# Kernel optimization log

Measured on AMD Instinct MI355X. Metric: run time of the kernel, lower is better.

Reference implementation:

```python
import jax, jax.numpy as jnp
import numpy as np
import math

N = 100000
D = 128       # input_dim
DK = 32       # d_k
H = 4         # heads
DV = D // H   # d_v = 32
DFF = 512     # 4 * input_dim
EPS = 1e-5


def layer_norm(x, g, b):
    mu = jnp.mean(x, axis=-1, keepdims=True)
    var = jnp.var(x, axis=-1, keepdims=True)
    return (x - mu) * jax.lax.rsqrt(var + EPS) * g + b


def setup_inputs() -> dict:
    key = jax.random.key(0)
    ks = jax.random.split(key, 10)
    x = jax.random.normal(ks[0], (N, D), dtype=jnp.float32)
    neighbor_index = jax.random.randint(ks[1], (N, 4), 0, N)
    # xavier-ish scaled params
    w_q = jax.random.normal(ks[2], (H, D, DK), dtype=jnp.float32) * math.sqrt(2.0 / (D + DK))
    w_k = jax.random.normal(ks[3], (H, 5, D, DK), dtype=jnp.float32) * math.sqrt(2.0 / (D + DK))
    w_v = jax.random.normal(ks[4], (H, 5, D, DV), dtype=jnp.float32) * math.sqrt(2.0 / (D + DV))
    W1 = jax.random.normal(ks[5], (D, DFF), dtype=jnp.float32) * math.sqrt(1.0 / D)
    b1 = jnp.zeros((DFF,), dtype=jnp.float32)
    W2 = jax.random.normal(ks[6], (DFF, D), dtype=jnp.float32) * math.sqrt(1.0 / DFF)
    b2 = jnp.zeros((D,), dtype=jnp.float32)
    g1 = jnp.ones((D,), dtype=jnp.float32)
    beta1 = jnp.zeros((D,), dtype=jnp.float32)
    g2 = jnp.ones((D,), dtype=jnp.float32)
    beta2 = jnp.zeros((D,), dtype=jnp.float32)
    return {"x": x, "neighbor_index": neighbor_index, "w_q": w_q, "w_k": w_k,
            "w_v": w_v, "W1": W1, "b1": b1, "W2": W2, "b2": b2,
            "g1": g1, "beta1": beta1, "g2": g2, "beta2": beta2}


def attention(x, neighbor_index, w_q, w_k, w_v):
    # gather the 4 typed neighbors and prepend the self node -> (N, 5, D)
    x_nb = jnp.concatenate([x[:, None, :], x[neighbor_index]], axis=1)
    Q = jnp.einsum('nd,hdk->hnk', x, w_q)                 # (H, N, DK)
    K = jnp.einsum('nrd,hrdk->hnrk', x_nb, w_k)           # (H, N, 5, DK)
    V = jnp.einsum('nrd,hrdv->hnrv', x_nb, w_v)           # (H, N, 5, DV)
    A = jnp.einsum('hnk,hnrk->hnr', Q, K) / math.sqrt(DK)
    # NOTE: original torch code applies softmax over dim=1 (the node axis),
    # reproduced faithfully here.
    A = jax.nn.softmax(A, axis=1)
    Z = jnp.einsum('hnr,hnrv->hnv', A, V)                 # (H, N, DV)
    return jnp.transpose(Z, (1, 0, 2)).reshape(x.shape[0], -1)  # (N, H*DV)


def reference(x, neighbor_index, w_q, w_k, w_v, W1, b1, W2, b2, g1, beta1, g2, beta2):
    attn = attention(x, neighbor_index, w_q, w_k, w_v)
    h = layer_norm(x + attn, g1, beta1)
    ffn = jax.nn.relu(h @ W1 + b1) @ W2 + b2
    return layer_norm(h + ffn, g2, beta2)
```

## Files before the change

kernel.cpp:

```cpp
#include <hip/hip_runtime.h>
#include <hip/hip_bf16.h>

typedef unsigned short u16;
typedef __attribute__((ext_vector_type(8))) short short8;
typedef __attribute__((ext_vector_type(4))) float f32x4;
typedef __attribute__((ext_vector_type(4))) float float4v;
typedef __attribute__((ext_vector_type(4))) unsigned short us4;
typedef __attribute__((ext_vector_type(4))) int int4v;

#define NN       100000
#define OFF_WK   16384
#define OFF_WV   98304
#define OFF_W1   180224
#define PACK_ELEMS 311296

#define WS_LWS   0u
#define WS_PM    8000000u
#define WS_PS    8000640u
#define WS_MHR   8001280u
#define WS_ISHR  8001408u
#define WS_PK    8001536u
#define WS_XB    8624128u
#define WS_SV    34224128u

#define PWS_PITCH 40
#define PWS_SLICE 1280

static __device__ __forceinline__ float b2f(u16 u){
  unsigned int i = ((unsigned int)u) << 16;
  float f; __builtin_memcpy(&f, &i, 4); return f;
}
static __device__ __forceinline__ u16 f2b(float f){
  unsigned int i; __builtin_memcpy(&i, &f, 4);
  i += 0x7FFFu + ((i >> 16) & 1u);
  return (u16)(i >> 16);
}
static __device__ __forceinline__ f32x4 mfma16(short8 a, short8 b, f32x4 c){
  return __builtin_amdgcn_mfma_f32_16x16x32_bf16(a, b, c, 0, 0, 0);
}
static __device__ __forceinline__ bool detect32(const void* g1){
  return ((const u16*)g1)[0] == 0;
}
static __device__ __forceinline__ float ldf(const void* p, size_t i, bool is32){
  return is32 ? ((const float*)p)[i] : b2f(((const u16*)p)[i]);
}

static __device__ __forceinline__ void stage32k(
    const u16* __restrict__ g, u16* l, int wv, int lane)
{
  #pragma unroll
  for (int k = 0; k < 8; k++){
    int off = k*4096 + wv*1024;
    __builtin_amdgcn_global_load_lds(
        (const __attribute__((address_space(1))) void*)((const char*)g + off + lane*16),
        (__attribute__((address_space(3))) void*)((char*)l + off),
        16, 0, 0);
  }
}

#define VMW8() asm volatile("s_waitcnt vmcnt(8)" ::: "memory")
#define VMW0() asm volatile("s_waitcnt vmcnt(0)" ::: "memory")
#define SBAR() asm volatile("s_barrier" ::: "memory")

__global__ __launch_bounds__(256) void k_convert_x(
    const void* __restrict__ x, const void* __restrict__ g1, u16* __restrict__ xb)
{
  const bool is32 = detect32(g1);
  size_t i = (size_t)blockIdx.x * 256 + threadIdx.x;
  us4 o;
  if (is32){
    float4v v = ((const float4v*)x)[i];
    o.x = f2b(v.x); o.y = f2b(v.y); o.z = f2b(v.z); o.w = f2b(v.w);
  } else {
    o = ((const us4*)x)[i];
  }
  ((us4*)xb)[i] = o;
}

__global__ __launch_bounds__(256) void k_pack(
    const void* __restrict__ wq, const void* __restrict__ wk,
    const void* __restrict__ wv, const void* __restrict__ W1,
    const void* __restrict__ W2, const void* __restrict__ g1,
    const void* __restrict__ b1, const void* __restrict__ b2,
    const void* __restrict__ be1, const void* __restrict__ g2,
    const void* __restrict__ be2,
    u16* __restrict__ pk, u16* __restrict__ sv)
{
  const bool is32 = detect32(g1);
  int p = blockIdx.x * 256 + threadIdx.x;
  if (p < PACK_ELEMS){
    float v;
    if (p < OFF_WK){
      int q = p;
      int j = q & 7, lane = (q >> 3) & 63, tk = q >> 9;
      int kb = tk & 3, t = tk >> 2;
      int kd = kb*32 + (lane>>4)*8 + j, nc = t*16 + (lane & 15);
      v = ldf(wq, (size_t)(nc>>5)*4096 + kd*32 + (nc & 31), is32);
    } else if (p < OFF_WV){
      int q = p - OFF_WK; int r = q >> 14; q &= 16383;
      int j = q & 7, lane = (q >> 3) & 63, tk = q >> 9;
      int kb = tk & 3, t = tk >> 2;
      int kd = kb*32 + (lane>>4)*8 + j, nc = t*16 + (lane & 15);
      v = ldf(wk, (size_t)((nc>>5)*5 + r)*4096 + kd*32 + (nc & 31), is32);
    } else if (p < OFF_W1){
      int q = p - OFF_WV; int r = q >> 14; q &= 16383;
      int j = q & 7, lane = (q >> 3) & 63, tk = q >> 9;
      int kb = tk & 3, t = tk >> 2;
      int kd = kb*32 + (lane>>4)*8 + j, nc = t*16 + (lane & 15);
      v = ldf(wv, (size_t)((nc>>5)*5 + r)*4096 + kd*32 + (nc & 31), is32);
    } else {
      int q = p - OFF_W1;
      int j = q & 7, lane = (q >> 3) & 63, rest = q >> 9;
      int pairIdx = rest >> 4, sub = rest & 15;
      int c = pairIdx >> 2, kb2 = pairIdx & 3;
      int half = lane >> 4, mc = lane & 15;
      if (sub < 8){
        int u = sub >> 2, kb = sub & 3;
        int kd = kb*32 + half*8 + j;
        int nc = c*128 + (kb2*2+u)*16 + mc;
        v = ldf(W1, (size_t)kd*512 + nc, is32);
      } else {
        int t = sub - 8;
        int kd = (c*4+kb2)*32 + half*8 + j;
        int nc = t*16 + mc;
        v = ldf(W2, (size_t)kd*128 + nc, is32);
      }
    }
    pk[p] = f2b(v);
  }
  if (blockIdx.x == 0){
    for (int i = threadIdx.x; i < 1152; i += 256){
      const void* src; int off;
      if      (i < 512) { src = b1;  off = i; }
      else if (i < 640) { src = b2;  off = i - 512; }
      else if (i < 768) { src = g1;  off = i - 640; }
      else if (i < 896) { src = be1; off = i - 768; }
      else if (i < 1024){ src = g2;  off = i - 896; }
      else              { src = be2; off = i - 1024; }
      sv[i] = f2b(ldf(src, off, is32));
    }
  }
}

__global__ __launch_bounds__(256, 2) void k_qk(
    const u16* __restrict__ x, const int* __restrict__ nbr,
    const u16* __restrict__ pw, float* __restrict__ lws)
{
  __shared__ __align__(16) u16 sbuf[32768];
  const int tid = threadIdx.x, lane = tid & 63, wv = tid >> 6;
  const int m = lane & 15, quad = lane >> 4;
  const int n0 = blockIdx.x * 128 + wv * 32;
  const bool act0 = (n0 < NN), act1 = (n0 + 16 < NN);
  const short8* sb8 = (const short8*)sbuf;

  int nd[2][4];
  short8 a2[2][4], a2n[2][4];
  #pragma unroll
  for (int tl = 0; tl < 2; tl++){
    if (!(tl ? act1 : act0)) continue;
    int4v t4 = *(const int4v*)(nbr + (size_t)(n0 + tl*16 + m)*4);
    nd[tl][0]=t4.x; nd[tl][1]=t4.y; nd[tl][2]=t4.z; nd[tl][3]=t4.w;
    const short8* xp = (const short8*)(x + (size_t)(n0 + tl*16 + m) * 128);
    #pragma unroll
    for (int kb = 0; kb < 4; kb++) a2[tl][kb] = xp[kb*4 + quad];
  }

  stage32k(pw, sbuf, wv, lane);
  stage32k(pw + OFF_WK, sbuf + 16384, wv, lane);

  f32x4 q[2][8];
  #pragma unroll
  for (int tl = 0; tl < 2; tl++)
    #pragma unroll
    for (int t = 0; t < 8; t++) q[tl][t] = (f32x4){0.f,0.f,0.f,0.f};

  VMW8(); SBAR();
  #pragma unroll
  for (int t = 0; t < 8; t++){
    short8 bfr[4];
    #pragma unroll
    for (int kb = 0; kb < 4; kb++) bfr[kb] = sb8[(t*4+kb)*64 + lane];
    #pragma unroll
    for (int tl = 0; tl < 2; tl++){
      if (!(tl ? act1 : act0)) continue;
      #pragma unroll
      for (int kb = 0; kb < 4; kb++) q[tl][t] = mfma16(a2[tl][kb], bfr[kb], q[tl][t]);
    }
  }
  SBAR();
  stage32k(pw + OFF_WK + 16384, sbuf, wv, lane);

  for (int r = 0; r < 5; r++){
    if (r < 4) { VMW8(); } else { VMW0(); }
    SBAR();
    const short8* cur = sb8 + ((r+1)&1)*2048;
    if (r < 4){
      #pragma unroll
      for (int tl = 0; tl < 2; tl++){
        if (!(tl ? act1 : act0)) continue;
        const short8* gp = (const short8*)(x + (size_t)nd[tl][r] * 128);
        #pragma unroll
        for (int kb = 0; kb < 4; kb++) a2n[tl][kb] = gp[kb*4 + quad];
      }
    }
    #pragma unroll
    for (int h = 0; h < 4; h++){
      short8 b0[4], b1f[4];
      #pragma unroll
      for (int kb = 0; kb < 4; kb++){
        b0[kb]  = cur[((2*h  )*4+kb)*64 + lane];
        b1f[kb] = cur[((2*h+1)*4+kb)*64 + lane];
      }
      #pragma unroll
      for (int tl = 0; tl < 2; tl++){
        if (!(tl ? act1 : act0)) continue;
        f32x4 k0 = {0.f,0.f,0.f,0.f}, k1 = {0.f,0.f,0.f,0.f};
        #pragma unroll
        for (int kb = 0; kb < 4; kb++){
          k0 = mfma16(a2[tl][kb], b0[kb],  k0);
          k1 = mfma16(a2[tl][kb], b1f[kb], k1);
        }
        float p[4];
        #pragma unroll
        for (int i = 0; i < 4; i++) p[i] = q[tl][2*h][i]*k0[i] + q[tl][2*h+1][i]*k1[i];
        #pragma unroll
        for (int mask = 1; mask < 16; mask <<= 1){
          #pragma unroll
          for (int i = 0; i < 4; i++) p[i] += __shfl_xor(p[i], mask, 16);
        }
        if (m == 0){
          #pragma unroll
          for (int i = 0; i < 4; i++)
            lws[(size_t)(h*5+r)*NN + n0 + tl*16 + quad*4 + i]
                = p[i] * 0.17677669529663687f;
        }
      }
    }
    if (r < 4){
      #pragma unroll
      for (int tl = 0; tl < 2; tl++)
        #pragma unroll
        for (int kb = 0; kb < 4; kb++) a2[tl][kb] = a2n[tl][kb];
    }
    SBAR();
    if (r <= 2)
      stage32k(pw + OFF_WK + (r+2)*16384, sbuf + ((r+1)&1)*16384, wv, lane);
  }
}

__global__ __launch_bounds__(256) void k_red_part(
    const float* __restrict__ lws, float* __restrict__ pm, float* __restrict__ ps)
{
  const int hr = blockIdx.x >> 3, pb = blockIdx.x & 7;
  const int start = pb * 12500, end = start + 12500;
  const float* v = lws + (size_t)hr * NN;
  __shared__ float red[256];
  float mx = -1e30f;
  for (int i = start + threadIdx.x; i < end; i += 256) mx = fmaxf(mx, v[i]);
  red[threadIdx.x] = mx; __syncthreads();
  for (int s = 128; s > 0; s >>= 1){
    if ((int)threadIdx.x < s) red[threadIdx.x] = fmaxf(red[threadIdx.x], red[threadIdx.x+s]);
    __syncthreads();
  }
  mx = red[0]; __syncthreads();
  float sm = 0.f;
  for (int i = start + threadIdx.x; i < end; i += 256) sm += __expf(v[i] - mx);
  red[threadIdx.x] = sm; __syncthreads();
  for (int s = 128; s > 0; s >>= 1){
    if ((int)threadIdx.x < s) red[threadIdx.x] += red[threadIdx.x+s];
    __syncthreads();
  }
  if (threadIdx.x == 0){ pm[blockIdx.x] = mx; ps[blockIdx.x] = red[0]; }
}

__global__ __launch_bounds__(64) void k_red_fin(
    const float* __restrict__ pm, const float* __restrict__ ps,
    float* __restrict__ mhr, float* __restrict__ ishr)
{
  int t = threadIdx.x;
  if (t < 20){
    float M = -1e30f;
    for (int b = 0; b < 8; b++) M = fmaxf(M, pm[t*8+b]);
    float S = 0.f;
    for (int b = 0; b < 8; b++) S += ps[t*8+b] * __expf(pm[t*8+b] - M);
    mhr[t] = M; ishr[t] = 1.0f / S;
  }
}

__global__ __launch_bounds__(256, 2) void k_attn_ffn(
    const u16* __restrict__ x, const void* __restrict__ xraw,
    const int* __restrict__ nbr,
    const u16* __restrict__ pw, const float* __restrict__ lws,
    const float* __restrict__ mhr, const float* __restrict__ ishr,
    const u16* __restrict__ sv, const void* __restrict__ g1raw,
    float* __restrict__ out)
{
  __shared__ __align__(16) u16 sbuf[32768];
  __shared__ __align__(16) u16 upool[5120];
  const int tid = threadIdx.x, lane = tid & 63, wv = tid >> 6;
  const int m = lane & 15, quad = lane >> 4;
  const int n0 = blockIdx.x * 128 + wv * 32;
  const bool act0 = (n0 < NN), act1 = (n0 + 16 < NN);
  const bool is32 = detect32(g1raw);
  const u16* b1s = sv;
  const u16* b2s = sv + 512;
  const u16* g1s = sv + 640;
  const u16* be1s = sv + 768;
  const u16* g2s = sv + 896;
  const u16* be2s = sv + 1024;
  const short8* sb8 = (const short8*)sbuf;
  float* attw_w = ((float*)upool) + wv * 640;
  u16*   pws_w  = upool + wv * PWS_SLICE;

  for (int j = lane; j < 640; j += 64){
    int tl = j / 320, rem = j - tl*320;
    int r = rem >> 6, h = (rem >> 4) & 3, mm = rem & 15, hr = h*5 + r;
    int node = n0 + tl*16 + mm;
    attw_w[j] = (node < NN)
        ? __expf(lws[(size_t)hr*NN + node] - mhr[hr]) * ishr[hr] : 0.f;
  }

  int nd[2][4];
  short8 a2[2][4], a2n[2][4];
  #pragma unroll
  for (int tl = 0; tl < 2; tl++){
    if (!(tl ? act1 : act0)) continue;
    int4v t4 = *(const int4v*)(nbr + (size_t)(n0 + tl*16 + m)*4);
    nd[tl][0]=t4.x; nd[tl][1]=t4.y; nd[tl][2]=t4.z; nd[tl][3]=t4.w;
    const short8* xp = (const short8*)(x + (size_t)(n0 + tl*16 + m) * 128);
    #pragma unroll
    for (int kb = 0; kb < 4; kb++) a2[tl][kb] = xp[kb*4 + quad];
  }

  stage32k(pw + OFF_WV, sbuf, wv, lane);
  stage32k(pw + OFF_WV + 16384, sbuf + 16384, wv, lane);

  f32x4 zacc[2][8];
  #pragma unroll
  for (int tl = 0; tl < 2; tl++)
    #pragma unroll
    for (int t = 0; t < 8; t++) zacc[tl][t] = (f32x4){0.f,0.f,0.f,0.f};

  for (int r = 0; r < 5; r++){
    VMW8(); SBAR();
    const short8* cur = sb8 + (r&1)*2048;
    if (r < 4){
      #pragma unroll
      for (int tl = 0; tl < 2; tl++){
        if (!(tl ? act1 : act0)) continue;
        const short8* gp = (const short8*)(x + (size_t)nd[tl][r] * 128);
        #pragma unroll
        for (int kb = 0; kb < 4; kb++) a2n[tl][kb] = gp[kb*4 + quad];
      }
    }
    #pragma unroll
    for (int t = 0; t < 8; t++){
      short8 bfr[4];
      #pragma unroll
      for (int kb = 0; kb < 4; kb++) bfr[kb] = cur[(t*4+kb)*64 + lane];
      int h = t >> 1;
      #pragma unroll
      for (int tl = 0; tl < 2; tl++){
        if (!(tl ? act1 : act0)) continue;
        f32x4 v = {0.f,0.f,0.f,0.f};
        #pragma unroll
        for (int kb = 0; kb < 4; kb++) v = mfma16(a2[tl][kb], bfr[kb], v);
        const float* aw = attw_w + tl*320 + (r*4+h)*16;
        #pragma unroll
        for (int i = 0; i < 4; i++) zacc[tl][t][i] += aw[quad*4+i] * v[i];
      }
    }
    if (r < 4){
      #pragma unroll
      for (int tl = 0; tl < 2; tl++)
        #pragma unroll
        for (int kb = 0; kb < 4; kb++) a2[tl][kb] = a2n[tl][kb];
    }
    SBAR();
    {
      int b = r + 2;
      const u16* src = (b < 5) ? pw + OFF_WV + b*16384
                               : pw + OFF_W1 + (b-5)*16384;
      stage32k(src, sbuf + (r&1)*16384, wv, lane);
    }
  }

  float mu[2][4], rs[2][4];
  #pragma unroll
  for (int tl = 0; tl < 2; tl++){
    if (!(tl ? act1 : act0)) continue;
    int rowb = n0 + tl*16;
    #pragma unroll
    for (int t = 0; t < 8; t++)
      #pragma unroll
      for (int i = 0; i < 4; i++)
        zacc[tl][t][i] += ldf(xraw, (size_t)(rowb + quad*4 + i)*128 + t*16 + m, is32);
    float s1[4] = {0,0,0,0}, s2[4] = {0,0,0,0};
    #pragma unroll
    for (int t = 0; t < 8; t++)
      #pragma unroll
      for (int i = 0; i < 4; i++){ float y = zacc[tl][t][i]; s1[i] += y; s2[i] += y*y; }
    #pragma unroll
    for (int mask = 1; mask < 16; mask <<= 1){
      #pragma unroll
      for (int i = 0; i < 4; i++){
        s1[i] += __shfl_xor(s1[i], mask, 16);
        s2[i] += __shfl_xor(s2[i], mask, 16);
      }
    }
    #pragma unroll
    for (int i = 0; i < 4; i++){
      mu[tl][i] = s1[i] * (1.f/128.f);
      float var = s2[i] * (1.f/128.f) - mu[tl][i]*mu[tl][i];
      rs[tl][i] = rsqrtf(var + 1e-5f);
    }
  }

  unsigned int hDp[2][8][2];
  short8 ah[2][4];
  #pragma unroll
  for (int kb = 0; kb < 4; kb++){
    #pragma unroll
    for (int u = 0; u < 2; u++){
      int t = kb*2 + u;
      #pragma unroll
      for (int tl = 0; tl < 2; tl++){
        if (!(tl ? act1 : act0)) continue;
        float gg = b2f(g1s[t*16+m]), bb = b2f(be1s[t*16+m]);
        u16 hv[4];
        #pragma unroll
        for (int i = 0; i < 4; i++){
          hv[i] = f2b((zacc[tl][t][i]-mu[tl][i])*rs[tl][i]*gg + bb);
          pws_w[(tl*16 + quad*4 + i)*PWS_PITCH + u*16 + m] = hv[i];
        }
        hDp[tl][t][0] = (unsigned int)hv[0] | ((unsigned int)hv[1] << 16);
        hDp[tl][t][1] = (unsigned int)hv[2] | ((unsigned int)hv[3] << 16);
      }
    }
    #pragma unroll
    for (int tl = 0; tl < 2; tl++)
      ah[tl][kb] = *(const short8*)(pws_w + (tl*16 + m)*PWS_PITCH + quad*8);
  }

  f32x4 f2acc[2][8];
  #pragma unroll
  for (int tl = 0; tl < 2; tl++)
    #pragma unroll
    for (int t = 0; t < 8; t++) f2acc[tl][t] = (f32x4){0.f,0.f,0.f,0.f};

  for (int s = 0; s < 8; s++){
    if (s < 7) { VMW8(); } else { VMW0(); }
    SBAR();
    const short8* cur = sb8 + ((s+1)&1)*2048;
    const int c = s >> 1, kp = s & 1;
    #pragma unroll
    for (int kb2w = 0; kb2w < 2; kb2w++){
      int kb2 = kp*2 + kb2w;
      const short8* w1f = cur + kb2w*1024;
      const short8* w2f = w1f + 512;
      #pragma unroll
      for (int u = 0; u < 2; u++){
        short8 bfr[4];
        #pragma unroll
        for (int kb = 0; kb < 4; kb++) bfr[kb] = w1f[(u*4+kb)*64 + lane];
        float b1c = b2f(b1s[c*128 + (kb2*2+u)*16 + m]);
        #pragma unroll
        for (int tl = 0; tl < 2; tl++){
          if (!(tl ? act1 : act0)) continue;
          f32x4 g = {0.f,0.f,0.f,0.f};
          #pragma unroll
          for (int kb = 0; kb < 4; kb++) g = mfma16(ah[tl][kb], bfr[kb], g);
          #pragma unroll
          for (int i = 0; i < 4; i++)
            pws_w[(tl*16 + quad*4 + i)*PWS_PITCH + u*16 + m]
                = f2b(fmaxf(g[i] + b1c, 0.f));
        }
      }
      short8 ag[2];
      #pragma unroll
      for (int tl = 0; tl < 2; tl++)
        ag[tl] = *(const short8*)(pws_w + (tl*16 + m)*PWS_PITCH + quad*8);
      #pragma unroll
      for (int t = 0; t < 8; t++){
        short8 bf = w2f[t*64 + lane];
        #pragma unroll
        for (int tl = 0; tl < 2; tl++){
          if (!(tl ? act1 : act0)) continue;
          f2acc[tl][t] = mfma16(ag[tl], bf, f2acc[tl][t]);
        }
      }
    }
    SBAR();
    if (s <= 5)
      stage32k(pw + OFF_W1 + (s+2)*16384, sbuf + ((s+1)&1)*16384, wv, lane);
  }

  #pragma unroll
  for (int tl = 0; tl < 2; tl++){
    if (!(tl ? act1 : act0)) continue;
    int rowb = n0 + tl*16;
    #pragma unroll
    for (int t = 0; t < 8; t++){
      float b2c = b2f(b2s[t*16 + m]);
      f2acc[tl][t][0] += b2f((u16)(hDp[tl][t][0] & 0xffff)) + b2c;
      f2acc[tl][t][1] += b2f((u16)(hDp[tl][t][0] >> 16))    + b2c;
      f2acc[tl][t][2] += b2f((u16)(hDp[tl][t][1] & 0xffff)) + b2c;
      f2acc[tl][t][3] += b2f((u16)(hDp[tl][t][1] >> 16))    + b2c;
    }
    float s1[4] = {0,0,0,0}, s2[4] = {0,0,0,0};
    #pragma unroll
    for (int t = 0; t < 8; t++)
      #pragma unroll
      for (int i = 0; i < 4; i++){ float y = f2acc[tl][t][i]; s1[i] += y; s2[i] += y*y; }
    #pragma unroll
    for (int mask = 1; mask < 16; mask <<= 1){
      #pragma unroll
      for (int i = 0; i < 4; i++){
        s1[i] += __shfl_xor(s1[i], mask, 16);
        s2[i] += __shfl_xor(s2[i], mask, 16);
      }
    }
    float mu2[4], rs2[4];
    #pragma unroll
    for (int i = 0; i < 4; i++){
      mu2[i] = s1[i] * (1.f/128.f);
      float var = s2[i] * (1.f/128.f) - mu2[i]*mu2[i];
      rs2[i] = rsqrtf(var + 1e-5f);
    }
    #pragma unroll
    for (int t = 0; t < 8; t++){
      float gg = b2f(g2s[t*16+m]), bb = b2f(be2s[t*16+m]);
      #pragma unroll
      for (int i = 0; i < 4; i++)
        out[(size_t)(rowb + quad*4 + i)*128 + t*16 + m] =
            (f2acc[tl][t][i]-mu2[i])*rs2[i]*gg + bb;
    }
  }
}

extern "C" void kernel_launch(void* const* d_in, const int* in_sizes, int n_in,
                              void* d_out, int out_size, void* d_ws, size_t ws_size,
                              hipStream_t stream)
{
  const void* x   = d_in[0];
  const int*  nbr = (const int*)d_in[1];
  const void* wq  = d_in[2];
  const void* wk  = d_in[3];
  const void* wv  = d_in[4];
  const void* W1  = d_in[5];
  const void* b1  = d_in[6];
  const void* W2  = d_in[7];
  const void* b2  = d_in[8];
  const void* g1  = d_in[9];
  const void* be1 = d_in[10];
  const void* g2  = d_in[11];
  const void* be2 = d_in[12];
  float* out = (float*)d_out;

  char* ws = (char*)d_ws;
  float* lws  = (float*)(ws + WS_LWS);
  float* pm   = (float*)(ws + WS_PM);
  float* ps   = (float*)(ws + WS_PS);
  float* mhr  = (float*)(ws + WS_MHR);
  float* ishr = (float*)(ws + WS_ISHR);
  u16*   pk   = (u16*)  (ws + WS_PK);
  u16*   xb   = (u16*)  (ws + WS_XB);
  u16*   sv   = (u16*)  (ws + WS_SV);

  k_convert_x<<<dim3(12500), dim3(256), 0, stream>>>(x, g1, xb);
  k_pack<<<dim3((PACK_ELEMS+255)/256), dim3(256), 0, stream>>>(wq, wk, wv, W1, W2, g1,
                                                               b1, b2, be1, g2, be2, pk, sv);
  k_qk<<<dim3((NN+127)/128), dim3(256), 0, stream>>>(xb, nbr, pk, lws);
  k_red_part<<<dim3(160), dim3(256), 0, stream>>>(lws, pm, ps);
  k_red_fin<<<dim3(1), dim3(64), 0, stream>>>(pm, ps, mhr, ishr);
  k_attn_ffn<<<dim3((NN+127)/128), dim3(256), 0, stream>>>(xb, x, nbr, pk, lws, mhr, ishr,
                                                           sv, g1, out);
}
```

Before: 306.0 us.

## Fuse prep kernels, fold final reduction into attention, swizzle workgroups, add MFMA priority

Merges the x-conversion and weight-packing kernels into one launch, and drops the single-block softmax finalize kernel by having each attention workgroup recompute the 20 global max/sum values into registers. Workgroup indices are remapped with an XCD-aware swizzle so that consecutive node tiles land on the same chiplet. s_setprio is raised around MFMA bursts, and the vmcnt waits are loosened so more prefetch loads can stay in flight. This removes two launches and their dependency gaps. The cost is redundant tiny reductions in every block and a risk around the relaxed wait counts.

```diff
diff --git a/kernel.cpp b/kernel.cpp
--- a/kernel.cpp
+++ b/kernel.cpp
@@ -9,6 +9,7 @@
 typedef __attribute__((ext_vector_type(4))) int int4v;
 
 #define NN       100000
+#define NWG      782
 #define OFF_WK   16384
 #define OFF_WV   98304
 #define OFF_W1   180224
@@ -44,6 +45,11 @@
 static __device__ __forceinline__ float ldf(const void* p, size_t i, bool is32){
   return is32 ? ((const float*)p)[i] : b2f(((const u16*)p)[i]);
 }
+static __device__ __forceinline__ int swz_wg(int b){
+  const int q = NWG >> 3, r = NWG & 7;
+  int x = b & 7, i = b >> 3;
+  return (x < r ? x*(q+1) : r*(q+1) + (x-r)*q) + i;
+}
 
 static __device__ __forceinline__ void stage32k(
     const u16* __restrict__ g, u16* l, int wv, int lane)
@@ -58,35 +64,34 @@
   }
 }
 
-#define VMW8() asm volatile("s_waitcnt vmcnt(8)" ::: "memory")
-#define VMW0() asm volatile("s_waitcnt vmcnt(0)" ::: "memory")
-#define SBAR() asm volatile("s_barrier" ::: "memory")
-
-__global__ __launch_bounds__(256) void k_convert_x(
-    const void* __restrict__ x, const void* __restrict__ g1, u16* __restrict__ xb)
+#define VMW16() asm volatile("s_waitcnt vmcnt(16)" ::: "memory")
+#define VMW8()  asm volatile("s_waitcnt vmcnt(8)" ::: "memory")
+#define VMW0()  asm volatile("s_waitcnt vmcnt(0)" ::: "memory")
+#define SBAR()  asm volatile("s_barrier" ::: "memory")
+#define PRIO1() __builtin_amdgcn_s_setprio(1)
+#define PRIO0() __builtin_amdgcn_s_setprio(0)
+
+__global__ __launch_bounds__(256) void k_prep(
+    const void* __restrict__ x, const void* __restrict__ wq,
+    const void* __restrict__ wk, const void* __restrict__ wv,
+    const void* __restrict__ W1, const void* __restrict__ W2,
+    const void* __restrict__ g1, const void* __restrict__ b1,
+    const void* __restrict__ b2, const void* __restrict__ be1,
+    const void* __restrict__ g2, const void* __restrict__ be2,
+    u16* __restrict__ xb, u16* __restrict__ pk, u16* __restrict__ sv)
 {
   const bool is32 = detect32(g1);
-  size_t i = (size_t)blockIdx.x * 256 + threadIdx.x;
-  us4 o;
-  if (is32){
-    float4v v = ((const float4v*)x)[i];
-    o.x = f2b(v.x); o.y = f2b(v.y); o.z = f2b(v.z); o.w = f2b(v.w);
-  } else {
-    o = ((const us4*)x)[i];
-  }
-  ((us4*)xb)[i] = o;
-}
-
-__global__ __launch_bounds__(256) void k_pack(
-    const void* __restrict__ wq, const void* __restrict__ wk,
-    const void* __restrict__ wv, const void* __restrict__ W1,
-    const void* __restrict__ W2, const void* __restrict__ g1,
-    const void* __restrict__ b1, const void* __restrict__ b2,
-    const void* __restrict__ be1, const void* __restrict__ g2,
-    const void* __restrict__ be2,
-    u16* __restrict__ pk, u16* __restrict__ sv)
-{
-  const bool is32 = detect32(g1);
+  {
+    size_t i = (size_t)blockIdx.x * 256 + threadIdx.x;
+    us4 o;
+    if (is32){
+      float4v v = ((const float4v*)x)[i];
+      o.x = f2b(v.x); o.y = f2b(v.y); o.z = f2b(v.z); o.w = f2b(v.w);
+    } else {
+      o = ((const us4*)x)[i];
+    }
+    ((us4*)xb)[i] = o;
+  }
   int p = blockIdx.x * 256 + threadIdx.x;
   if (p < PACK_ELEMS){
     float v;
@@ -149,7 +154,8 @@
   __shared__ __align__(16) u16 sbuf[32768];
   const int tid = threadIdx.x, lane = tid & 63, wv = tid >> 6;
   const int m = lane & 15, quad = lane >> 4;
-  const int n0 = blockIdx.x * 128 + wv * 32;
+  const int blk = swz_wg(blockIdx.x);
+  const int n0 = blk * 128 + wv * 32;
   const bool act0 = (n0 < NN), act1 = (n0 + 16 < NN);
   const short8* sb8 = (const short8*)sbuf;
 
@@ -175,6 +181,7 @@
     for (int t = 0; t < 8; t++) q[tl][t] = (f32x4){0.f,0.f,0.f,0.f};
 
   VMW8(); SBAR();
+  PRIO1();
   #pragma unroll
   for (int t = 0; t < 8; t++){
     short8 bfr[4];
@@ -187,11 +194,12 @@
       for (int kb = 0; kb < 4; kb++) q[tl][t] = mfma16(a2[tl][kb], bfr[kb], q[tl][t]);
     }
   }
+  PRIO0();
   SBAR();
   stage32k(pw + OFF_WK + 16384, sbuf, wv, lane);
 
   for (int r = 0; r < 5; r++){
-    if (r < 4) { VMW8(); } else { VMW0(); }
+    if (r >= 1 && r <= 3) { VMW16(); } else { VMW8(); }
     SBAR();
     const short8* cur = sb8 + ((r+1)&1)*2048;
     if (r < 4){
@@ -215,11 +223,13 @@
       for (int tl = 0; tl < 2; tl++){
         if (!(tl ? act1 : act0)) continue;
         f32x4 k0 = {0.f,0.f,0.f,0.f}, k1 = {0.f,0.f,0.f,0.f};
+        PRIO1();
         #pragma unroll
         for (int kb = 0; kb < 4; kb++){
           k0 = mfma16(a2[tl][kb], b0[kb],  k0);
           k1 = mfma16(a2[tl][kb], b1f[kb], k1);
         }
+        PRIO0();
         float p[4];
         #pragma unroll
         for (int i = 0; i < 4; i++) p[i] = q[tl][2*h][i]*k0[i] + q[tl][2*h+1][i]*k1[i];
@@ -273,25 +283,11 @@
   if (threadIdx.x == 0){ pm[blockIdx.x] = mx; ps[blockIdx.x] = red[0]; }
 }
 
-__global__ __launch_bounds__(64) void k_red_fin(
-    const float* __restrict__ pm, const float* __restrict__ ps,
-    float* __restrict__ mhr, float* __restrict__ ishr)
-{
-  int t = threadIdx.x;
-  if (t < 20){
-    float M = -1e30f;
-    for (int b = 0; b < 8; b++) M = fmaxf(M, pm[t*8+b]);
-    float S = 0.f;
-    for (int b = 0; b < 8; b++) S += ps[t*8+b] * __expf(pm[t*8+b] - M);
-    mhr[t] = M; ishr[t] = 1.0f / S;
-  }
-}
-
 __global__ __launch_bounds__(256, 2) void k_attn_ffn(
     const u16* __restrict__ x, const void* __restrict__ xraw,
     const int* __restrict__ nbr,
     const u16* __restrict__ pw, const float* __restrict__ lws,
-    const float* __restrict__ mhr, const float* __restrict__ ishr,
+    const float* __restrict__ pm, const float* __restrict__ ps,
     const u16* __restrict__ sv, const void* __restrict__ g1raw,
     float* __restrict__ out)
 {
@@ -299,7 +295,8 @@
   __shared__ __align__(16) u16 upool[5120];
   const int tid = threadIdx.x, lane = tid & 63, wv = tid >> 6;
   const int m = lane & 15, quad = lane >> 4;
-  const int n0 = blockIdx.x * 128 + wv * 32;
+  const int blk = swz_wg(blockIdx.x);
+  const int n0 = blk * 128 + wv * 32;
   const bool act0 = (n0 < NN), act1 = (n0 + 16 < NN);
   const bool is32 = detect32(g1raw);
   const u16* b1s = sv;
@@ -309,15 +306,29 @@
   const u16* g2s = sv + 896;
   const u16* be2s = sv + 1024;
   const short8* sb8 = (const short8*)sbuf;
+  const u16* wvp = pw + OFF_WV;
+  const u16* wfp = pw + OFF_W1;
   float* attw_w = ((float*)upool) + wv * 640;
   u16*   pws_w  = upool + wv * PWS_SLICE;
+
+  float Mreg = -1e30f, iSreg = 0.f;
+  if (lane < 20){
+    float M = -1e30f;
+    #pragma unroll
+    for (int b = 0; b < 8; b++) M = fmaxf(M, pm[lane*8+b]);
+    float S = 0.f;
+    #pragma unroll
+    for (int b = 0; b < 8; b++) S += ps[lane*8+b] * __expf(pm[lane*8+b] - M);
+    Mreg = M; iSreg = 1.0f / S;
+  }
 
   for (int j = lane; j < 640; j += 64){
     int tl = j / 320, rem = j - tl*320;
     int r = rem >> 6, h = (rem >> 4) & 3, mm = rem & 15, hr = h*5 + r;
     int node = n0 + tl*16 + mm;
+    float Mh = __shfl(Mreg, hr), iSh = __shfl(iSreg, hr);
     attw_w[j] = (node < NN)
-        ? __expf(lws[(size_t)hr*NN + node] - mhr[hr]) * ishr[hr] : 0.f;
+        ? __expf(lws[(size_t)hr*NN + node] - Mh) * iSh : 0.f;
   }
 
   int nd[2][4];
@@ -332,8 +343,8 @@
     for (int kb = 0; kb < 4; kb++) a2[tl][kb] = xp[kb*4 + quad];
   }
 
-  stage32k(pw + OFF_WV, sbuf, wv, lane);
-  stage32k(pw + OFF_WV + 16384, sbuf + 16384, wv, lane);
+  stage32k(wvp, sbuf, wv, lane);
+  stage32k(wvp + 16384, sbuf + 16384, wv, lane);
 
   f32x4 zacc[2][8];
   #pragma unroll
@@ -342,7 +353,8 @@
     for (int t = 0; t < 8; t++) zacc[tl][t] = (f32x4){0.f,0.f,0.f,0.f};
 
   for (int r = 0; r < 5; r++){
-    VMW8(); SBAR();
+    if (r >= 1) { VMW16(); } else { VMW8(); }
+    SBAR();
     const short8* cur = sb8 + (r&1)*2048;
     if (r < 4){
       #pragma unroll
@@ -363,8 +375,10 @@
       for (int tl = 0; tl < 2; tl++){
         if (!(tl ? act1 : act0)) continue;
         f32x4 v = {0.f,0.f,0.f,0.f};
+        PRIO1();
         #pragma unroll
         for (int kb = 0; kb < 4; kb++) v = mfma16(a2[tl][kb], bfr[kb], v);
+        PRIO0();
         const float* aw = attw_w + tl*320 + (r*4+h)*16;
         #pragma unroll
         for (int i = 0; i < 4; i++) zacc[tl][t][i] += aw[quad*4+i] * v[i];
@@ -379,8 +393,7 @@
     SBAR();
     {
       int b = r + 2;
-      const u16* src = (b < 5) ? pw + OFF_WV + b*16384
-                               : pw + OFF_W1 + (b-5)*16384;
+      const u16* src = (b < 5) ? wvp + b*16384 : wfp + (b-5)*16384;
       stage32k(src, sbuf + (r&1)*16384, wv, lane);
     }
   }
@@ -468,8 +481,10 @@
         for (int tl = 0; tl < 2; tl++){
           if (!(tl ? act1 : act0)) continue;
           f32x4 g = {0.f,0.f,0.f,0.f};
+          PRIO1();
           #pragma unroll
           for (int kb = 0; kb < 4; kb++) g = mfma16(ah[tl][kb], bfr[kb], g);
+          PRIO0();
           #pragma unroll
           for (int i = 0; i < 4; i++)
             pws_w[(tl*16 + quad*4 + i)*PWS_PITCH + u*16 + m]
@@ -480,6 +495,7 @@
       #pragma unroll
       for (int tl = 0; tl < 2; tl++)
         ag[tl] = *(const short8*)(pws_w + (tl*16 + m)*PWS_PITCH + quad*8);
+      PRIO1();
       #pragma unroll
       for (int t = 0; t < 8; t++){
         short8 bf = w2f[t*64 + lane];
@@ -489,10 +505,11 @@
           f2acc[tl][t] = mfma16(ag[tl], bf, f2acc[tl][t]);
         }
       }
+      PRIO0();
     }
     SBAR();
     if (s <= 5)
-      stage32k(pw + OFF_W1 + (s+2)*16384, sbuf + ((s+1)&1)*16384, wv, lane);
+      stage32k(wfp + (s+2)*16384, sbuf + ((s+1)&1)*16384, wv, lane);
   }
 
   #pragma unroll
@@ -561,18 +578,14 @@
   float* lws  = (float*)(ws + WS_LWS);
   float* pm   = (float*)(ws + WS_PM);
   float* ps   = (float*)(ws + WS_PS);
-  float* mhr  = (float*)(ws + WS_MHR);
-  float* ishr = (float*)(ws + WS_ISHR);
   u16*   pk   = (u16*)  (ws + WS_PK);
   u16*   xb   = (u16*)  (ws + WS_XB);
   u16*   sv   = (u16*)  (ws + WS_SV);
 
-  k_convert_x<<<dim3(12500), dim3(256), 0, stream>>>(x, g1, xb);
-  k_pack<<<dim3((PACK_ELEMS+255)/256), dim3(256), 0, stream>>>(wq, wk, wv, W1, W2, g1,
-                                                               b1, b2, be1, g2, be2, pk, sv);
-  k_qk<<<dim3((NN+127)/128), dim3(256), 0, stream>>>(xb, nbr, pk, lws);
+  k_prep<<<dim3(12500), dim3(256), 0, stream>>>(x, wq, wk, wv, W1, W2, g1,
+                                                b1, b2, be1, g2, be2, xb, pk, sv);
+  k_qk<<<dim3(NWG), dim3(256), 0, stream>>>(xb, nbr, pk, lws);
   k_red_part<<<dim3(160), dim3(256), 0, stream>>>(lws, pm, ps);
-  k_red_fin<<<dim3(1), dim3(64), 0, stream>>>(pm, ps, mhr, ishr);
-  k_attn_ffn<<<dim3((NN+127)/128), dim3(256), 0, stream>>>(xb, x, nbr, pk, lws, mhr, ishr,
-                                                           sv, g1, out);
-}
+  k_attn_ffn<<<dim3(NWG), dim3(256), 0, stream>>>(xb, x, nbr, pk, lws, pm, ps,
+                                                  sv, g1, out);
+}
```

Measured after the change: 297.5 us. 2.8% less time.
